# Kernel optimization log

Measured on AMD Instinct MI355X. Metric: run time of the kernel, lower is better.

Reference implementation:

```python
import jax, jax.numpy as jnp
import numpy as np

N, F, E, WID, M, K = 100000, 128, 128, 4, 25000, 16
HID = WID * F    # width * num_features = 512
DHID = WID * E   # discriminator hidden = 512
EPS = 1e-5


def _v2v(x, v_idx, w_e):
    """Hypergraph v2v mean aggregation: v->e mean (scaled by w_e), then e->v mean."""
    Mm, Kk = v_idx.shape
    C = x.shape[1]
    ef = jnp.zeros((Mm, C), x.dtype)
    for k in range(Kk):  # K is small and static; avoids a [M,K,C] materialization
        ef = ef + x[v_idx[:, k]]
    ef = ef * (w_e / Kk)[:, None]  # weighted edge features [M, C]
    out = jnp.zeros_like(x)
    deg = jnp.zeros((x.shape[0],), x.dtype)
    for k in range(Kk):
        out = out.at[v_idx[:, k]].add(ef)
        deg = deg.at[v_idx[:, k]].add(1.0)
    return out / jnp.maximum(deg, 1.0)[:, None]


def _bn(h, g, bt):
    # BatchNorm1d in training mode: biased batch stats over vertex dim
    m = h.mean(0)
    v = ((h - m) ** 2).mean(0)
    return g * (h - m) * jax.lax.rsqrt(v + EPS) + bt


def _conv(x, Wt, b, g, bt, v_idx, w_e, last=False):
    h = _bn(x @ Wt.T + b, g, bt)
    h = _v2v(h, v_idx, w_e)
    return h if last else jax.nn.relu(h)  # dropout = identity (eval mode)


def setup_inputs() -> dict:
    key = jax.random.key(0)
    ks = iter(jax.random.split(key, 64))

    def lin(o, i):
        s = 1.0 / np.sqrt(i)
        return (jax.random.uniform(next(ks), (o, i), minval=-s, maxval=s, dtype=jnp.float32),
                jax.random.uniform(next(ks), (o,), minval=-s, maxval=s, dtype=jnp.float32))

    d = {}
    d["X"] = jax.random.normal(next(ks), (N, F), dtype=jnp.float32)
    d["v_idx"] = jax.random.randint(next(ks), (M, K), 0, N, dtype=jnp.int32)
    d["w_e"] = jax.random.uniform(next(ks), (M,), dtype=jnp.float32)
    for name, (o, i) in [("enc1", (HID, F)), ("enc2", (E, HID)), ("fc", (E, HID)),
                         ("f1u", (E, E)), ("f2u", (E, E)), ("f1r", (E, E)), ("f2r", (E, E)),
                         ("f1", (E, E)), ("f2", (E, E)),
                         ("dis1", (DHID, E)), ("dis2", (2, DHID)),
                         ("dec1", (HID, E)), ("dec2", (F, HID))]:
        Wt, b = lin(o, i)
        d[name + "_W"] = Wt
        d[name + "_b"] = b
    for name, c in [("enc1", HID), ("enc2", E), ("dis1", DHID), ("dis2", 2), ("dec1", HID), ("dec2", F)]:
        d[name + "_g"] = jnp.ones((c,), jnp.float32)
        d[name + "_bt"] = jnp.zeros((c,), jnp.float32)
    return d


def reference(X, v_idx, w_e,
              enc1_W, enc1_b, enc2_W, enc2_b, fc_W, fc_b,
              f1u_W, f1u_b, f2u_W, f2u_b, f1r_W, f1r_b, f2r_W, f2r_b,
              f1_W, f1_b, f2_W, f2_b,
              dis1_W, dis1_b, dis2_W, dis2_b, dec1_W, dec1_b, dec2_W, dec2_b,
              enc1_g, enc1_bt, enc2_g, enc2_bt, dis1_g, dis1_bt, dis2_g, dis2_bt,
              dec1_g, dec1_bt, dec2_g, dec2_bt):
    # encoder (returns last output and first-layer output)
    x1 = _conv(X, enc1_W, enc1_b, enc1_g, enc1_bt, v_idx, w_e)            # [N, HID]
    xe = _conv(x1, enc2_W, enc2_b, enc2_g, enc2_bt, v_idx, w_e, last=True)  # [N, E]
    xe1 = x1 @ fc_W.T + fc_b                                               # [N, E]
    # GRU-style gating
    z = jax.nn.sigmoid(xe1 @ f1u_W.T + f1u_b + xe @ f2u_W.T + f2u_b)
    r = jax.nn.sigmoid(xe1 @ f1r_W.T + f1r_b + xe @ f2r_W.T + f2r_b)
    o = jnp.tanh(xe1 @ f1_W.T + f1_b + (r * xe) @ f2_W.T + f2_b)
    outs = z * o + (1.0 - z) * xe                                          # [N, E]
    # attention pooling (n = input_size - 1)
    dd = (outs - outs.mean(0)) ** 2
    vv = dd.sum(0) / (N - 1)
    ee = dd / (4.0 * (vv + 0.001)) + 0.5
    proto = (outs * jax.nn.sigmoid(ee)).sum(0)                             # [E]
    # gradient reversal is identity in the forward pass
    h = _conv(outs, dis1_W, dis1_b, dis1_g, dis1_bt, v_idx, w_e)
    xdis = _conv(h, dis2_W, dis2_b, dis2_g, dis2_bt, v_idx, w_e, last=True)  # [N, 2]
    h = _conv(outs, dec1_W, dec1_b, dec1_g, dec1_bt, v_idx, w_e)
    x_de = _conv(h, dec2_W, dec2_b, dec2_g, dec2_bt, v_idx, w_e, last=True)  # [N, F]
    return (outs, x_de, proto, xdis)
```

## Files before the change

### kernel.cpp

```cpp
#include <hip/hip_runtime.h>
#include <cstddef>
#include <cstdint>

static constexpr int NV = 100000;
static constexpr int NP = 100096;
static constexpr int ME = 25000;
static constexpr int MEP = 25088;
static constexpr int KE = 16;
static constexpr float BN_EPS = 1e-5f;

typedef unsigned int u32;
typedef __attribute__((ext_vector_type(8))) short s16x8;
typedef __attribute__((ext_vector_type(8))) unsigned short u16x8;
typedef __attribute__((ext_vector_type(4))) float f32x4;

__device__ __forceinline__ float sigm(float x) { return 1.0f / (1.0f + expf(-x)); }
__device__ __forceinline__ float bf2f(unsigned short u) {
    union { u32 i; float f; } v; v.i = ((u32)u) << 16; return v.f;
}
__device__ __forceinline__ unsigned short f2bf(float f) {
    union { float f; u32 i; } v; v.f = f;
    u32 u = v.i;
    return (unsigned short)((u + 0x7FFFu + ((u >> 16) & 1u)) >> 16);
}

#define GLD16(g, l) __builtin_amdgcn_global_load_lds(                          \
    (__attribute__((address_space(1))) const unsigned int*)(g),                \
    (__attribute__((address_space(3))) unsigned int*)(l), 16, 0, 0)

#define STAGE_A(b, k0)                                                         \
  {                                                                            \
    unsigned short* sA_ = sm + (b) * 8192;                                     \
    _Pragma("unroll")                                                          \
    for (int i_ = 0; i_ < 4; ++i_) {                                           \
      const unsigned short* g_ = A + (size_t)(bm + 32 * w + 8 * i_ + (l >> 3)) * IC + (k0) + swz; \
      GLD16(g_, sA_ + 2048 * w + 512 * i_);                                    \
    }                                                                          \
  }

__global__ __launch_bounds__(256)
void mfma_gemm(const unsigned short* __restrict__ A, int IC,
               const unsigned short* __restrict__ W, const float* __restrict__ bias,
               unsigned short* __restrict__ Cb, int ldb, int cb0,
               unsigned short* __restrict__ Cb2, int ldb2, int splitN,
               float* __restrict__ s1f, float* __restrict__ s2f, int statsC)
{
    __shared__ unsigned short sm[2 * 8192];
    const int BX = gridDim.x;
    const int total = BX * gridDim.y;
    const int flat = blockIdx.x + BX * blockIdx.y;
    const int q = total >> 3, r = total & 7;
    const int xcd = flat & 7, sub = flat >> 3;
    const int base = (xcd < r) ? xcd * (q + 1) : r * (q + 1) + (xcd - r) * q;
    const int vid = base + sub;
    const int bm = (vid / BX) * 128;
    const int bn = (vid % BX) * 64;

    const int tid = threadIdx.x;
    const int l = tid & 63, w = tid >> 6;
    const int wrow = w >> 1, wcol = w & 1;

    f32x4 acc[4][2];
    #pragma unroll
    for (int m = 0; m < 4; ++m)
        #pragma unroll
        for (int n = 0; n < 2; ++n)
            #pragma unroll
            for (int r2 = 0; r2 < 4; ++r2) acc[m][n][r2] = 0.f;

    const int swz = (((l & 7) ^ (l >> 3)) << 3);
    const int nt = IC >> 6;

    STAGE_A(0, 0);
    asm volatile("s_waitcnt vmcnt(0)" ::: "memory");
    __builtin_amdgcn_s_barrier();

    for (int t = 0; t < nt; ++t) {
        const int cur = t & 1;
        if (t + 1 < nt) STAGE_A(cur ^ 1, (t + 1) << 6);
        const unsigned short* sA = sm + cur * 8192;
        #pragma unroll
        for (int ks = 0; ks < 2; ++ks) {
            const int koff = ks * 32 + ((l >> 4) << 3);
            s16x8 afr[4], bfr[2];
            #pragma unroll
            for (int m = 0; m < 4; ++m) {
                int row = wrow * 64 + m * 16 + (l & 15);
                afr[m] = *(const s16x8*)&sA[row * 64 + (koff ^ ((l & 7) << 3))];
            }
            #pragma unroll
            for (int n = 0; n < 2; ++n) {
                int col = bn + wcol * 32 + n * 16 + (l & 15);
                bfr[n] = *(const s16x8*)&W[(size_t)col * IC + (t << 6) + koff];
            }
            #pragma unroll
            for (int m = 0; m < 4; ++m)
                #pragma unroll
                for (int n = 0; n < 2; ++n)
                    acc[m][n] = __builtin_amdgcn_mfma_f32_16x16x32_bf16(
                        afr[m], bfr[n], acc[m][n], 0, 0, 0);
        }
        asm volatile("s_waitcnt vmcnt(0)" ::: "memory");
        __builtin_amdgcn_s_barrier();
    }

    unsigned short* dst = Cb;
    int ld = ldb, co = cb0;
    if (Cb2 && bn >= splitN) { dst = Cb2; ld = ldb2; co = -splitN; }

    #pragma unroll
    for (int n = 0; n < 2; ++n) {
        const int col = bn + wcol * 32 + n * 16 + (l & 15);
        const float bs = bias[col];
        float ssum = 0.f, sq = 0.f;
        #pragma unroll
        for (int m = 0; m < 4; ++m) {
            const int row0 = bm + wrow * 64 + m * 16 + ((l >> 4) << 2);
            #pragma unroll
            for (int r2 = 0; r2 < 4; ++r2) {
                float v = acc[m][n][r2] + bs;
                int row = row0 + r2;
                if (dst) dst[(size_t)row * ld + co + col] = f2bf(v);
                if (s1f && col < statsC && row < NV) { ssum += v; sq += v * v; }
            }
        }
        if (s1f && col < statsC) {
            ssum += __shfl_xor(ssum, 16); ssum += __shfl_xor(ssum, 32);
            sq   += __shfl_xor(sq, 16);   sq   += __shfl_xor(sq, 32);
            if ((l >> 4) == 0) {
                atomicAdd(&s1f[col], ssum);
                atomicAdd(&s2f[col], sq);
            }
        }
    }
}

__global__ __launch_bounds__(256)
void mfma_gemm_ef2(const unsigned short* __restrict__ A,
                   const unsigned short* __restrict__ W,
                   const float* __restrict__ we,
                   const float* __restrict__ P, const float* __restrict__ Q,
                   unsigned short* __restrict__ ef0, unsigned short* __restrict__ ef1)
{
    const int IC = 128;
    __shared__ unsigned short sm[2 * 8192];
    const int bm = blockIdx.y * 128;
    const int bn = blockIdx.x * 64;
    const int tid = threadIdx.x;
    const int l = tid & 63, w = tid >> 6;
    const int wrow = w >> 1, wcol = w & 1;

    f32x4 acc[4][2];
    #pragma unroll
    for (int m = 0; m < 4; ++m)
        #pragma unroll
        for (int n = 0; n < 2; ++n)
            #pragma unroll
            for (int r = 0; r < 4; ++r) acc[m][n][r] = 0.f;

    const int swz = (((l & 7) ^ (l >> 3)) << 3);

    STAGE_A(0, 0);
    asm volatile("s_waitcnt vmcnt(0)" ::: "memory");
    __builtin_amdgcn_s_barrier();

    #pragma unroll
    for (int t = 0; t < 2; ++t) {
        const int cur = t & 1;
        if (t == 0) STAGE_A(1, 64);
        const unsigned short* sA = sm + cur * 8192;
        #pragma unroll
        for (int ks = 0; ks < 2; ++ks) {
            const int koff = ks * 32 + ((l >> 4) << 3);
            s16x8 afr[4], bfr[2];
            #pragma unroll
            for (int m = 0; m < 4; ++m) {
                int row = wrow * 64 + m * 16 + (l & 15);
                afr[m] = *(const s16x8*)&sA[row * 64 + (koff ^ ((l & 7) << 3))];
            }
            #pragma unroll
            for (int n = 0; n < 2; ++n) {
                int col = bn + wcol * 32 + n * 16 + (l & 15);
                bfr[n] = *(const s16x8*)&W[(size_t)col * 128 + (t << 6) + koff];
            }
            #pragma unroll
            for (int m = 0; m < 4; ++m)
                #pragma unroll
                for (int n = 0; n < 2; ++n)
                    acc[m][n] = __builtin_amdgcn_mfma_f32_16x16x32_bf16(
                        afr[m], bfr[n], acc[m][n], 0, 0, 0);
        }
        asm volatile("s_waitcnt vmcnt(0)" ::: "memory");
        __builtin_amdgcn_s_barrier();
    }

    unsigned short* dst = (bn < 512) ? ef0 : ef1;
    const int co = (bn < 512) ? 0 : -512;

    #pragma unroll
    for (int n = 0; n < 2; ++n) {
        const int colg = bn + wcol * 32 + n * 16 + (l & 15);
        const float pc = P[colg], qc = Q[colg];
        #pragma unroll
        for (int m = 0; m < 4; ++m) {
            const int row0 = bm + wrow * 64 + m * 16 + ((l >> 4) << 2);
            #pragma unroll
            for (int r = 0; r < 4; ++r) {
                int row = row0 + r;
                if (row < ME) {
                    float wv = we[row];
                    dst[(size_t)row * 512 + co + colg] = f2bf(wv * (pc * acc[m][n][r] + qc));
                }
            }
        }
    }
}

__global__ __launch_bounds__(256)
void cov_kernel(const unsigned short* __restrict__ A, float* __restrict__ cov)
{
    __shared__ unsigned short T[128 * 64];
    const int tid = threadIdx.x;
    const int l = tid & 63, w = tid >> 6;

    f32x4 acc[2][8];
    #pragma unroll
    for (int m = 0; m < 2; ++m)
        #pragma unroll
        for (int n = 0; n < 8; ++n)
            #pragma unroll
            for (int r = 0; r < 4; ++r) acc[m][n][r] = 0.f;

    const int r0 = blockIdx.x * 1024;
    for (int ch = 0; ch < 16; ++ch) {
        const int rbase = r0 + ch * 64;
        __syncthreads();
        #pragma unroll
        for (int q = 0; q < 4; ++q) {
            int idx = tid + q * 256;
            int r = idx & 63, cg = idx >> 6;
            int row = rbase + r;
            u16x8 u = {0, 0, 0, 0, 0, 0, 0, 0};
            if (row < NV) u = *(const u16x8*)&A[(size_t)row * 128 + cg * 8];
            #pragma unroll
            for (int j = 0; j < 8; ++j) {
                int c = cg * 8 + j;
                T[c * 64 + (r ^ ((c & 7) << 3))] = u[j];
            }
        }
        __syncthreads();
        #pragma unroll
        for (int ks = 0; ks < 2; ++ks) {
            const int koff = ks * 32 + ((l >> 4) << 3);
            s16x8 fi[2], fj[8];
            #pragma unroll
            for (int m = 0; m < 2; ++m) {
                int c = (w * 2 + m) * 16 + (l & 15);
                fi[m] = *(const s16x8*)&T[c * 64 + (koff ^ ((c & 7) << 3))];
            }
            #pragma unroll
            for (int n = 0; n < 8; ++n) {
                int c = n * 16 + (l & 15);
                fj[n] = *(const s16x8*)&T[c * 64 + (koff ^ ((c & 7) << 3))];
            }
            #pragma unroll
            for (int m = 0; m < 2; ++m)
                #pragma unroll
                for (int n = 0; n < 8; ++n)
                    acc[m][n] = __builtin_amdgcn_mfma_f32_16x16x32_bf16(
                        fi[m], fj[n], acc[m][n], 0, 0, 0);
        }
    }
    #pragma unroll
    for (int m = 0; m < 2; ++m) {
        #pragma unroll
        for (int n = 0; n < 8; ++n) {
            #pragma unroll
            for (int r = 0; r < 4; ++r) {
                int row = (w * 2 + m) * 16 + ((l >> 4) << 2) + r;
                int col = n * 16 + (l & 15);
                atomicAdd(&cov[row * 128 + col], acc[m][n][r]);
            }
        }
    }
}

__global__ __launch_bounds__(128)
void quadform_kernel(const float* __restrict__ cov, const float* __restrict__ colsum,
                     const unsigned short* __restrict__ Wt, const float* __restrict__ bias,
                     float* __restrict__ s1, float* __restrict__ s2)
{
    const int c = blockIdx.x, i = threadIdx.x;
    __shared__ float wv[128];
    __shared__ float red[128][2];
    float wi = bf2f(Wt[c * 128 + i]);
    wv[i] = wi;
    __syncthreads();
    const float* crow = cov + i * 128;
    float dot = 0.f;
    #pragma unroll 8
    for (int j = 0; j < 128; ++j) dot += crow[j] * wv[j];
    red[i][0] = wi * dot;
    red[i][1] = wi * colsum[i];
    __syncthreads();
    for (int s = 64; s > 0; s >>= 1) {
        if (i < s) { red[i][0] += red[i + s][0]; red[i][1] += red[i + s][1]; }
        __syncthreads();
    }
    if (i == 0) {
        float b = bias[c];
        float ws = red[0][1];
        s1[c] = ws + (float)NV * b;
        s2[c] = red[0][0] + 2.f * b * ws + (float)NV * b * b;
    }
}

__global__ void prep_weights(const float* e1, const float* e2, const float* fcw,
                             const float* d1, const float* dc1, const float* dc2,
                             const float* ds2,
                             const float* f1u, const float* f2u,
                             const float* f1r, const float* f2r,
                             const float* f1, const float* f2,
                             const float* f1ub, const float* f2ub,
                             const float* f1rb, const float* f2rb,
                             const float* f1b, const float* f2b,
                             const float* ds1b, const float* dc1b,
                             const float* e2b, const float* fcb,
                             unsigned short* WB, float* bzr, float* bo,
                             float* bdd, float* bef)
{
    int i = blockIdx.x * 256 + threadIdx.x;
    if (i < 65536)           WB[i] = f2bf(e1[i]);
    else if (i < 131072)     WB[i] = f2bf(e2[i - 65536]);
    else if (i < 196608)     WB[i] = f2bf(fcw[i - 131072]);
    else if (i < 262144)     WB[i] = f2bf(d1[i - 196608]);
    else if (i < 327680)     WB[i] = f2bf(dc1[i - 262144]);
    else if (i < 393216)     WB[i] = f2bf(dc2[i - 327680]);
    else if (i < 394240)     WB[i] = f2bf(ds2[i - 393216]);
    else if (i < 459776) {
        int j = i - 394240, row = j >> 8, c = j & 255;
        float v;
        if (row < 128) v = (c < 128) ? f1u[row * 128 + c] : f2u[row * 128 + c - 128];
        else { int rr = row - 128; v = (c < 128) ? f1r[rr * 128 + c] : f2r[rr * 128 + c - 128]; }
        WB[i] = f2bf(v);
    } else if (i < 492544) {
        int j = i - 459776, row = j >> 8, c = j & 255;
        float v = (c < 128) ? f1[row * 128 + c] : f2[row * 128 + c - 128];
        WB[i] = f2bf(v);
    } else if (i < 492800) {
        int o = i - 492544;
        bzr[o] = (o < 128) ? (f1ub[o] + f2ub[o]) : (f1rb[o - 128] + f2rb[o - 128]);
    } else if (i < 492928) {
        int o = i - 492800;
        bo[o] = f1b[o] + f2b[o];
    } else if (i < 493952) {
        int o = i - 492928;
        bdd[o] = (o < 512) ? ds1b[o] : dc1b[o - 512];
    } else if (i < 494208) {
        int o = i - 493952;
        bef[o] = (o < 128) ? e2b[o] : fcb[o - 128];
    }
}

__global__ void cvt_f32_bf16(const float* __restrict__ in, unsigned short* __restrict__ out, int n)
{
    int i = (blockIdx.x * 256 + threadIdx.x) * 4;
    if (i < n) {
        float4 v = *reinterpret_cast<const float4*>(&in[i]);
        out[i] = f2bf(v.x); out[i + 1] = f2bf(v.y);
        out[i + 2] = f2bf(v.z); out[i + 3] = f2bf(v.w);
    }
}

__global__ void bn_finalize_kernel(const float* __restrict__ s1, const float* __restrict__ s2,
                                   const float* __restrict__ g, const float* __restrict__ bt,
                                   float* __restrict__ scale, float* __restrict__ shift,
                                   int C, float invN)
{
    int c = threadIdx.x;
    if (c < C) {
        float m = s1[c] * invN;
        float v = fmaxf(s2[c] * invN - m * m, 0.f);
        float sc = g[c] * rsqrtf(v + BN_EPS);
        scale[c] = sc;
        shift[c] = bt[c] - m * sc;
    }
}

__global__ void bn_finalize_pq(const float* __restrict__ s1, const float* __restrict__ s2,
                               const float* __restrict__ g, const float* __restrict__ bt,
                               const float* __restrict__ bias,
                               float* __restrict__ P, float* __restrict__ Q,
                               int C, int off, float invN)
{
    int c = threadIdx.x;
    if (c < C) {
        int cc = off + c;
        float m = s1[cc] * invN;
        float v = fmaxf(s2[cc] * invN - m * m, 0.f);
        float sc = g[c] * rsqrtf(v + BN_EPS);
        float sh = bt[c] - m * sc;
        P[cc] = sc * (1.0f / KE);
        Q[cc] = sc * bias[c] + sh;
    }
}

__global__ __launch_bounds__(256)
void edge_gather_sum(const unsigned short* __restrict__ x, const int* __restrict__ vidx,
                     unsigned short* __restrict__ ge)
{
    const int e = blockIdx.x * 16 + (threadIdx.x >> 4);
    const int cp = (threadIdx.x & 15) << 3;
    if (e >= ME) return;
    float s[8] = {};
    const int* vi = vidx + e * KE;
    #pragma unroll
    for (int k = 0; k < KE; ++k) {
        int v = vi[k];
        u16x8 u = *(const u16x8*)&x[(size_t)v * 128 + cp];
        #pragma unroll
        for (int j = 0; j < 8; ++j) s[j] += bf2f(u[j]);
    }
    u16x8 o;
    #pragma unroll
    for (int j = 0; j < 8; ++j) o[j] = f2bf(s[j]);
    *(u16x8*)&ge[(size_t)e * 128 + cp] = o;
}

__global__ __launch_bounds__(256)
void edge_gather_bf(const unsigned short* __restrict__ pre, const int* __restrict__ vidx,
                    const float* __restrict__ we, const float* __restrict__ scl,
                    const float* __restrict__ shf, unsigned short* __restrict__ ef, int C)
{
    const int tpe = C >> 3;
    const int epb = 256 / tpe;
    const int e = blockIdx.x * epb + threadIdx.x / tpe;
    const int cp = (threadIdx.x % tpe) << 3;
    if (e >= ME) return;
    float s[8] = {};
    const int* vi = vidx + e * KE;
    #pragma unroll
    for (int k = 0; k < KE; ++k) {
        int v = vi[k];
        u16x8 u = *(const u16x8*)&pre[(size_t)v * C + cp];
        #pragma unroll
        for (int j = 0; j < 8; ++j) s[j] += bf2f(u[j]);
    }
    float wv = we[e] * (1.0f / KE);
    u16x8 o;
    #pragma unroll
    for (int j = 0; j < 8; ++j)
        o[j] = f2bf(wv * (scl[cp + j] * s[j] + (float)KE * shf[cp + j]));
    *(u16x8*)&ef[(size_t)e * C + cp] = o;
}

__global__ void edge_gather2_kernel(const float* __restrict__ X, const int* __restrict__ vidx,
                                    const float* __restrict__ we, const float* __restrict__ scale,
                                    const float* __restrict__ shift, float* __restrict__ ef)
{
    int e = blockIdx.x * blockDim.x + threadIdx.x;
    if (e >= ME) return;
    float s0 = 0.f, s1v = 0.f;
    #pragma unroll
    for (int k = 0; k < KE; ++k) {
        int v = vidx[e * KE + k];
        s0 += X[2 * v];
        s1v += X[2 * v + 1];
    }
    float w = we[e] * (1.0f / KE);
    ef[2 * e]     = w * (scale[0] * s0 + (float)KE * shift[0]);
    ef[2 * e + 1] = w * (scale[1] * s1v + (float)KE * shift[1]);
}

__global__ void deg_kernel(const int* __restrict__ vidx, int* __restrict__ deg)
{
    int i = blockIdx.x * blockDim.x + threadIdx.x;
    if (i < ME * KE) atomicAdd(&deg[vidx[i]], 1);
}

__global__ void scan_block_kernel(const int* __restrict__ deg, int* __restrict__ rowptr,
                                  int* __restrict__ blocksums, int n)
{
    __shared__ int tmp[256];
    int i = blockIdx.x * 256 + threadIdx.x;
    int v = (i < n) ? deg[i] : 0;
    tmp[threadIdx.x] = v;
    __syncthreads();
    for (int off = 1; off < 256; off <<= 1) {
        int t = (threadIdx.x >= off) ? tmp[threadIdx.x - off] : 0;
        __syncthreads();
        tmp[threadIdx.x] += t;
        __syncthreads();
    }
    if (i < n) rowptr[i] = tmp[threadIdx.x] - v;
    if (threadIdx.x == 255) blocksums[blockIdx.x] = tmp[255];
}

__global__ void scan_sums_par(int* __restrict__ bs, int nb)
{
    __shared__ int tmp[512];
    int t = threadIdx.x;
    int v = (t < nb) ? bs[t] : 0;
    tmp[t] = v;
    __syncthreads();
    for (int off = 1; off < 512; off <<= 1) {
        int u = (t >= off) ? tmp[t - off] : 0;
        __syncthreads();
        tmp[t] += u;
        __syncthreads();
    }
    if (t < nb) bs[t] = tmp[t] - v;
}

__global__ void scan_add_kernel(int* __restrict__ rowptr, const int* __restrict__ blocksums, int n)
{
    int i = blockIdx.x * 256 + threadIdx.x;
    if (i < n) rowptr[i] += blocksums[blockIdx.x];
    if (i == 0) rowptr[n] = ME * KE;
}

__global__ void csr_fill_kernel(const int* __restrict__ vidx, int* __restrict__ cursor,
                                int* __restrict__ csr)
{
    int i = blockIdx.x * blockDim.x + threadIdx.x;
    if (i < ME * KE) {
        int v = vidx[i];
        int pos = atomicAdd(&cursor[v], 1);
        csr[pos] = i >> 4;
    }
}

__global__ __launch_bounds__(256)
void csr_gather_bf(const unsigned short* __restrict__ ef, int ldE, int cb0E,
                   const int* __restrict__ rowptr, const int* __restrict__ csr,
                   float* __restrict__ outf, int ldf,
                   unsigned short* __restrict__ outb, int ldb, int cb0,
                   unsigned short* __restrict__ outb2, int ldb2,
                   int C, int relu)
{
    const int lpv = C >> 3;
    const int vpb = 256 / lpv;
    const int v = blockIdx.x * vpb + threadIdx.x / lpv;
    const int lg = threadIdx.x % lpv;
    if (v >= NV) return;
    const int s = rowptr[v], e = rowptr[v + 1];
    float a[8] = {};
    int i = s;
    for (; i + 2 <= e; i += 2) {
        int e0 = csr[i], e1 = csr[i + 1];
        u16x8 u0 = *(const u16x8*)&ef[(size_t)e0 * ldE + cb0E + lg * 8];
        u16x8 u1 = *(const u16x8*)&ef[(size_t)e1 * ldE + cb0E + lg * 8];
        #pragma unroll
        for (int j = 0; j < 8; ++j) a[j] += bf2f(u0[j]) + bf2f(u1[j]);
    }
    if (i < e) {
        int e0 = csr[i];
        u16x8 u0 = *(const u16x8*)&ef[(size_t)e0 * ldE + cb0E + lg * 8];
        #pragma unroll
        for (int j = 0; j < 8; ++j) a[j] += bf2f(u0[j]);
    }
    float inv = 1.0f / (float)max(e - s, 1);
    #pragma unroll
    for (int j = 0; j < 8; ++j) {
        float x = a[j] * inv;
        if (relu) x = fmaxf(x, 0.f);
        a[j] = x;
    }
    if (outf) {
        float* p = outf + (size_t)v * ldf + lg * 8;
        #pragma unroll
        for (int j = 0; j < 8; ++j) p[j] = a[j];
    }
    if (outb) {
        u16x8 o;
        #pragma unroll
        for (int j = 0; j < 8; ++j) o[j] = f2bf(a[j]);
        *(u16x8*)&outb[(size_t)v * ldb + cb0 + lg * 8] = o;
    }
    if (outb2) {
        u16x8 o;
        #pragma unroll
        for (int j = 0; j < 8; ++j) o[j] = f2bf(a[j]);
        *(u16x8*)&outb2[(size_t)v * ldb2 + lg * 8] = o;
    }
}

__global__ __launch_bounds__(256)
void csr_gather_dis(const unsigned short* __restrict__ ef,
                    const int* __restrict__ rowptr, const int* __restrict__ csr,
                    const unsigned short* __restrict__ wdis2, const float* __restrict__ dis2b,
                    float* __restrict__ pre22)
{
    const int w = threadIdx.x >> 6, l = threadIdx.x & 63;
    const int v = blockIdx.x * 4 + w;
    if (v >= NV) return;
    const int s = rowptr[v], e = rowptr[v + 1];
    float a[8] = {};
    int i = s;
    for (; i + 2 <= e; i += 2) {
        int e0 = csr[i], e1 = csr[i + 1];
        u16x8 u0 = *(const u16x8*)&ef[(size_t)e0 * 512 + l * 8];
        u16x8 u1 = *(const u16x8*)&ef[(size_t)e1 * 512 + l * 8];
        #pragma unroll
        for (int j = 0; j < 8; ++j) a[j] += bf2f(u0[j]) + bf2f(u1[j]);
    }
    if (i < e) {
        int e0 = csr[i];
        u16x8 u0 = *(const u16x8*)&ef[(size_t)e0 * 512 + l * 8];
        #pragma unroll
        for (int j = 0; j < 8; ++j) a[j] += bf2f(u0[j]);
    }
    float inv = 1.0f / (float)max(e - s, 1);
    u16x8 w0 = *(const u16x8*)&wdis2[l * 8];
    u16x8 w1 = *(const u16x8*)&wdis2[512 + l * 8];
    float d0 = 0.f, d1 = 0.f;
    #pragma unroll
    for (int j = 0; j < 8; ++j) {
        float h = fmaxf(a[j] * inv, 0.f);
        d0 += h * bf2f(w0[j]);
        d1 += h * bf2f(w1[j]);
    }
    for (int o = 32; o > 0; o >>= 1) {
        d0 += __shfl_down(d0, o);
        d1 += __shfl_down(d1, o);
    }
    if (l == 0) {
        pre22[2 * v]     = d0 + dis2b[0];
        pre22[2 * v + 1] = d1 + dis2b[1];
    }
}

__global__ void csr_gather2_kernel(const float* __restrict__ ef, const int* __restrict__ rowptr,
                                   const int* __restrict__ csr, float* __restrict__ outp)
{
    int v = blockIdx.x * blockDim.x + threadIdx.x;
    if (v >= NV) return;
    int s = rowptr[v], e = rowptr[v + 1];
    float a0 = 0.f, a1 = 0.f;
    for (int i = s; i < e; ++i) {
        int ed = csr[i];
        a0 += ef[2 * ed];
        a1 += ef[2 * ed + 1];
    }
    float inv = 1.0f / (float)max(e - s, 1);
    outp[2 * v]     = a0 * inv;
    outp[2 * v + 1] = a1 * inv;
}

__global__ __launch_bounds__(256)
void colstats_bf(const unsigned short* __restrict__ Xb,
                 float* __restrict__ s1, float* __restrict__ s2)
{
    const int t = threadIdx.x;
    const int cg = t & 15;
    const int rs = t >> 4;
    float s[8] = {}, q[8] = {};
    for (int r = blockIdx.x * 16 + rs; r < NV; r += 256 * 16) {
        u16x8 u = *(const u16x8*)&Xb[(size_t)r * 128 + cg * 8];
        #pragma unroll
        for (int j = 0; j < 8; ++j) {
            float v = bf2f(u[j]);
            s[j] += v; q[j] += v * v;
        }
    }
    __shared__ float ls[16][16][8];
    __shared__ float lq[16][16][8];
    #pragma unroll
    for (int j = 0; j < 8; ++j) { ls[rs][cg][j] = s[j]; lq[rs][cg][j] = q[j]; }
    __syncthreads();
    int c = t & 127;
    float a = 0.f;
    if (t < 128) {
        #pragma unroll
        for (int i = 0; i < 16; ++i) a += ls[i][c >> 3][c & 7];
        atomicAdd(&s1[c], a);
    } else {
        #pragma unroll
        for (int i = 0; i < 16; ++i) a += lq[i][c >> 3][c & 7];
        atomicAdd(&s2[c], a);
    }
}

__global__ void att_finalize_kernel(const float* __restrict__ s1, const float* __restrict__ s2,
                                    float* __restrict__ mu, float* __restrict__ qd, int C)
{
    int c = threadIdx.x;
    if (c < C) {
        float m = s1[c] / (float)NV;
        float vv = fmaxf((s2[c] - (float)NV * m * m) / (float)(NV - 1), 0.f);
        mu[c] = m;
        qd[c] = 1.0f / (4.0f * (vv + 0.001f));
    }
}

__global__ __launch_bounds__(256)
void proto_ws(const float* __restrict__ outsf, const float* __restrict__ mu,
              const float* __restrict__ qd, float* __restrict__ proto)
{
    const int t = threadIdx.x;
    const int cg = t & 31;
    const int rs = t >> 5;
    const float4* X4 = (const float4*)outsf;
    const float4 m = ((const float4*)mu)[cg];
    const float4 q = ((const float4*)qd)[cg];
    float4 acc = make_float4(0.f, 0.f, 0.f, 0.f);
    for (int r = blockIdx.x * 8 + rs; r < NV; r += 256 * 8) {
        float4 x = X4[(size_t)r * 32 + cg];
        float d0 = (x.x - m.x) * (x.x - m.x);
        float d1 = (x.y - m.y) * (x.y - m.y);
        float d2 = (x.z - m.z) * (x.z - m.z);
        float d3 = (x.w - m.w) * (x.w - m.w);
        acc.x += x.x * sigm(d0 * q.x + 0.5f);
        acc.y += x.y * sigm(d1 * q.y + 0.5f);
        acc.z += x.z * sigm(d2 * q.z + 0.5f);
        acc.w += x.w * sigm(d3 * q.w + 0.5f);
    }
    __shared__ float4 ls[8][32];
    ls[rs][cg] = acc;
    __syncthreads();
    if (t < 128) {
        float a = 0.f;
        #pragma unroll
        for (int i = 0; i < 8; ++i) {
            const float* f = (const float*)&ls[i][t >> 2];
            a += f[t & 3];
        }
        atomicAdd(&proto[t], a);
    }
}

__global__ void colstats2_kernel(const float* __restrict__ X, int N,
                                 float* __restrict__ s1, float* __restrict__ s2)
{
    __shared__ float red[256][4];
    int t = threadIdx.x;
    float a0 = 0, a1 = 0, b0 = 0, b1 = 0;
    for (int r = blockIdx.x * 256 + t; r < N; r += 256 * gridDim.x) {
        float x0 = X[2 * r], x1 = X[2 * r + 1];
        a0 += x0; b0 += x0 * x0;
        a1 += x1; b1 += x1 * x1;
    }
    red[t][0] = a0; red[t][1] = a1; red[t][2] = b0; red[t][3] = b1;
    __syncthreads();
    for (int s = 128; s > 0; s >>= 1) {
        if (t < s)
            for (int j = 0; j < 4; ++j) red[t][j] += red[t + s][j];
        __syncthreads();
    }
    if (t == 0) {
        atomicAdd(&s1[0], red[0][0]);
        atomicAdd(&s1[1], red[0][1]);
        atomicAdd(&s2[0], red[0][2]);
        atomicAdd(&s2[1], red[0][3]);
    }
}

__global__ void rx_kernel(const unsigned short* __restrict__ ZR, const unsigned short* __restrict__ xeb,
                          unsigned short* __restrict__ G, int n8)
{
    int idx = blockIdx.x * blockDim.x + threadIdx.x;
    if (idx >= n8) return;
    int i8 = idx * 8;
    int row = i8 >> 7, c = i8 & 127;
    u16x8 rv = *(const u16x8*)&ZR[(size_t)row * 256 + 128 + c];
    u16x8 xv = *(const u16x8*)&xeb[i8];
    u16x8 g;
    #pragma unroll
    for (int j = 0; j < 8; ++j)
        g[j] = f2bf(sigm(bf2f(rv[j])) * bf2f(xv[j]));
    *(u16x8*)&G[(size_t)row * 256 + 128 + c] = g;
}

__global__ void gru_out_kernel(const unsigned short* __restrict__ ZR, const unsigned short* __restrict__ Opre,
                               const unsigned short* __restrict__ xeb,
                               float* __restrict__ outs, unsigned short* __restrict__ outsb,
                               float* __restrict__ outsf, int n8)
{
    int idx = blockIdx.x * blockDim.x + threadIdx.x;
    if (idx >= n8) return;
    int i8 = idx * 8;
    int row = i8 >> 7, c = i8 & 127;
    u16x8 zv = *(const u16x8*)&ZR[(size_t)row * 256 + c];
    u16x8 ov = *(const u16x8*)&Opre[i8];
    u16x8 xv = *(const u16x8*)&xeb[i8];
    float val[8];
    u16x8 ob;
    #pragma unroll
    for (int j = 0; j < 8; ++j) {
        float z = sigm(bf2f(zv[j]));
        float o = tanhf(bf2f(ov[j]));
        float xe = bf2f(xv[j]);
        val[j] = z * o + (1.f - z) * xe;
        ob[j] = f2bf(val[j]);
    }
    *(float4*)&outs[i8]     = make_float4(val[0], val[1], val[2], val[3]);
    *(float4*)&outs[i8 + 4] = make_float4(val[4], val[5], val[6], val[7]);
    *(float4*)&outsf[i8]     = make_float4(val[0], val[1], val[2], val[3]);
    *(float4*)&outsf[i8 + 4] = make_float4(val[4], val[5], val[6], val[7]);
    *(u16x8*)&outsb[i8] = ob;
}

extern "C" void kernel_launch(void* const* d_in, const int* in_sizes, int n_in,
                              void* d_out, int out_size, void* d_ws, size_t ws_size,
                              hipStream_t stream)
{
    const float* X      = (const float*)d_in[0];
    const int*   vidx   = (const int*)  d_in[1];
    const float* we     = (const float*)d_in[2];
    const float* enc1_W = (const float*)d_in[3];  const float* enc1_b = (const float*)d_in[4];
    const float* enc2_W = (const float*)d_in[5];  const float* enc2_b = (const float*)d_in[6];
    const float* fc_W   = (const float*)d_in[7];  const float* fc_b   = (const float*)d_in[8];
    const float* f1u_W  = (const float*)d_in[9];  const float* f1u_b  = (const float*)d_in[10];
    const float* f2u_W  = (const float*)d_in[11]; const float* f2u_b  = (const float*)d_in[12];
    const float* f1r_W  = (const float*)d_in[13]; const float* f1r_b  = (const float*)d_in[14];
    const float* f2r_W  = (const float*)d_in[15]; const float* f2r_b  = (const float*)d_in[16];
    const float* f1_W   = (const float*)d_in[17]; const float* f1_b   = (const float*)d_in[18];
    const float* f2_W   = (const float*)d_in[19]; const float* f2_b   = (const float*)d_in[20];
    const float* dis1_W = (const float*)d_in[21]; const float* dis1_b = (const float*)d_in[22];
    const float* dis2_W = (const float*)d_in[23]; const float* dis2_b = (const float*)d_in[24];
    const float* dec1_W = (const float*)d_in[25]; const float* dec1_b = (const float*)d_in[26];
    const float* dec2_W = (const float*)d_in[27]; const float* dec2_b = (const float*)d_in[28];
    const float* enc1_g = (const float*)d_in[29]; const float* enc1_bt = (const float*)d_in[30];
    const float* enc2_g = (const float*)d_in[31]; const float* enc2_bt = (const float*)d_in[32];
    const float* dis1_g = (const float*)d_in[33]; const float* dis1_bt = (const float*)d_in[34];
    const float* dis2_g = (const float*)d_in[35]; const float* dis2_bt = (const float*)d_in[36];
    const float* dec1_g = (const float*)d_in[37]; const float* dec1_bt = (const float*)d_in[38];
    const float* dec2_g = (const float*)d_in[39]; const float* dec2_bt = (const float*)d_in[40];

    float* out   = (float*)d_out;
    float* outs  = out;
    float* x_de  = out + 12800000;
    float* proto = out + 25600000;
    float* xdis  = out + 25600128;

    char* base = (char*)d_ws;
    unsigned short* bufA = (unsigned short*)base;
    char* p = base + (size_t)NP * 512 * 2;
    unsigned short* bufE = (unsigned short*)p; p += (size_t)MEP * 1024 * 2;
    unsigned short* Greg = (unsigned short*)p;
    unsigned short* Xbf  = Greg;
    unsigned short* outsb = Greg + (size_t)NP * 128;
    p += (size_t)NP * 256 * 2;
    unsigned short* x1bf = (unsigned short*)p; p += (size_t)NP * 512 * 2;
    unsigned short* WB = (unsigned short*)p; p += 492544 * 2 + 1024;
    float* bzr = (float*)p; p += 256 * 4;
    float* bo  = (float*)p; p += 128 * 4;
    float* bdd = (float*)p; p += 1024 * 4;
    float* bef = (float*)p; p += 256 * 4;
    float* s1  = (float*)p; p += 1024 * 4;
    float* s2  = (float*)p; p += 1024 * 4;
    float* scl = (float*)p; p += 1024 * 4;
    float* shf = (float*)p; p += 1024 * 4;
    float* sX1 = (float*)p; p += 128 * 4;
    float* sX2 = (float*)p; p += 128 * 4;
    float* sA1 = (float*)p; p += 128 * 4;
    float* sA2 = (float*)p; p += 128 * 4;
    float* covX = (float*)p; p += 16384 * 4;
    float* covA = (float*)p; p += 16384 * 4;
    int* deg    = (int*)p; p += (size_t)NV * 4;
    int* rowptr = (int*)p; p += (size_t)(NV + 1) * 4;
    int* cursor = (int*)p; p += (size_t)NV * 4;
    int* bsums  = (int*)p; p += 512 * 4;
    int* csr    = (int*)p; p += (size_t)ME * KE * 4;
    float* outsf = (float*)p; p += (size_t)NP * 128 * 4;
    unsigned short* ge = (unsigned short*)p;

    unsigned short* bufE0 = bufE;
    unsigned short* bufE1 = bufE + (size_t)MEP * 512;

    unsigned short* pre128 = bufA;
    unsigned short* xe_bf  = bufA + (size_t)NP * 128;
    unsigned short* ZR     = bufA + (size_t)NP * 256;
    unsigned short* Opre   = bufA;
    unsigned short* hdec   = bufA;
    float* pre22 = (float*)(Greg + (size_t)NP * 128);
    float* bufEf = (float*)bufE;

    unsigned short* wenc1 = WB;
    unsigned short* wenc2 = WB + 65536;
    unsigned short* wdd   = WB + 196608;
    unsigned short* wdec2 = WB + 327680;
    unsigned short* wdis2 = WB + 393216;
    unsigned short* wzr   = WB + 394240;
    unsigned short* wo    = WB + 459776;

    const int n128 = NV * 128;
    const int n8 = n128 / 8;
    const int nScanBlocks = (NV + 255) / 256;

    auto gemm = [&](const unsigned short* A, int ic, const unsigned short* W, const float* b,
                    unsigned short* Cb, int ldb, int cb0,
                    unsigned short* Cb2, int ldb2, int splitN,
                    int oc, float* st1, float* st2, int statsC) {
        dim3 g(oc / 64, NP / 128);
        mfma_gemm<<<g, 256, 0, stream>>>(A, ic, W, b, Cb, ldb, cb0, Cb2, ldb2, splitN,
                                         st1, st2, statsC);
    };

    prep_weights<<<1931, 256, 0, stream>>>(enc1_W, enc2_W, fc_W, dis1_W, dec1_W, dec2_W, dis2_W,
                                           f1u_W, f2u_W, f1r_W, f2r_W, f1_W, f2_W,
                                           f1u_b, f2u_b, f1r_b, f2r_b, f1_b, f2_b,
                                           dis1_b, dec1_b, enc2_b, fc_b,
                                           WB, bzr, bo, bdd, bef);
    cvt_f32_bf16<<<(n128 / 4 + 255) / 256, 256, 0, stream>>>(X, Xbf, n128);

    hipMemsetAsync(deg, 0, NV * sizeof(int), stream);
    deg_kernel<<<(ME * KE + 255) / 256, 256, 0, stream>>>(vidx, deg);
    scan_block_kernel<<<nScanBlocks, 256, 0, stream>>>(deg, rowptr, bsums, NV);
    scan_sums_par<<<1, 512, 0, stream>>>(bsums, nScanBlocks);
    scan_add_kernel<<<nScanBlocks, 256, 0, stream>>>(rowptr, bsums, NV);
    hipMemcpyAsync(cursor, rowptr, NV * sizeof(int), hipMemcpyDeviceToDevice, stream);
    csr_fill_kernel<<<(ME * KE + 255) / 256, 256, 0, stream>>>(vidx, cursor, csr);

    hipMemsetAsync(sX1, 0, 256 * sizeof(float), stream);
    hipMemsetAsync(covX, 0, 16384 * sizeof(float), stream);
    colstats_bf<<<256, 256, 0, stream>>>(Xbf, sX1, sX2);
    cov_kernel<<<98, 256, 0, stream>>>(Xbf, covX);
    quadform_kernel<<<512, 128, 0, stream>>>(covX, sX1, wenc1, enc1_b, s1, s2);
    bn_finalize_pq<<<1, 512, 0, stream>>>(s1, s2, enc1_g, enc1_bt, enc1_b, scl, shf, 512, 0, 1.0f / NV);
    edge_gather_sum<<<(ME + 15) / 16, 256, 0, stream>>>(Xbf, vidx, ge);
    { dim3 g(8, MEP / 128);
      mfma_gemm_ef2<<<g, 256, 0, stream>>>(ge, wenc1, we, scl, shf, bufE0, bufE1); }
    csr_gather_bf<<<NV / 4, 256, 0, stream>>>(bufE0, 512, 0, rowptr, csr,
        nullptr, 0, x1bf, 512, 0, nullptr, 0, 512, 1);

    hipMemsetAsync(s1, 0, 2048 * sizeof(float), stream);
    gemm(x1bf, 512, wenc2, bef, pre128, 128, 0, Greg, 256, 128, 256, s1, s2, 128);
    bn_finalize_kernel<<<1, 512, 0, stream>>>(s1, s2, enc2_g, enc2_bt, scl, shf, 128, 1.0f / NV);
    edge_gather_bf<<<(ME + 15) / 16, 256, 0, stream>>>(pre128, vidx, we, scl, shf, bufE0, 128);
    csr_gather_bf<<<NV / 16, 256, 0, stream>>>(bufE0, 128, 0, rowptr, csr,
        nullptr, 0, Greg, 256, 128, xe_bf, 128, 128, 0);

    gemm(Greg, 256, wzr, bzr, ZR, 256, 0, nullptr, 0, 1 << 30, 256, nullptr, nullptr, 0);
    rx_kernel<<<(n8 + 255) / 256, 256, 0, stream>>>(ZR, xe_bf, Greg, n8);
    gemm(Greg, 256, wo, bo, Opre, 128, 0, nullptr, 0, 1 << 30, 128, nullptr, nullptr, 0);
    gru_out_kernel<<<(n8 + 255) / 256, 256, 0, stream>>>(ZR, Opre, xe_bf, outs, outsb, outsf, n8);

    hipMemsetAsync(sA1, 0, 256 * sizeof(float), stream);
    colstats_bf<<<256, 256, 0, stream>>>(outsb, sA1, sA2);
    att_finalize_kernel<<<1, 128, 0, stream>>>(sA1, sA2, scl, shf, 128);
    hipMemsetAsync(proto, 0, 128 * sizeof(float), stream);
    proto_ws<<<256, 256, 0, stream>>>(outsf, scl, shf, proto);

    hipMemsetAsync(covA, 0, 16384 * sizeof(float), stream);
    cov_kernel<<<98, 256, 0, stream>>>(outsb, covA);
    quadform_kernel<<<1024, 128, 0, stream>>>(covA, sA1, wdd, bdd, s1, s2);
    bn_finalize_pq<<<1, 512, 0, stream>>>(s1, s2, dis1_g, dis1_bt, dis1_b, scl, shf, 512, 0, 1.0f / NV);
    bn_finalize_pq<<<1, 512, 0, stream>>>(s1, s2, dec1_g, dec1_bt, dec1_b, scl, shf, 512, 512, 1.0f / NV);
    edge_gather_sum<<<(ME + 15) / 16, 256, 0, stream>>>(outsb, vidx, ge);
    { dim3 g(16, MEP / 128);
      mfma_gemm_ef2<<<g, 256, 0, stream>>>(ge, wdd, we, scl, shf, bufE0, bufE1); }
    csr_gather_dis<<<NV / 4, 256, 0, stream>>>(bufE0, rowptr, csr, wdis2, dis2_b, pre22);
    csr_gather_bf<<<NV / 4, 256, 0, stream>>>(bufE1, 512, 0, rowptr, csr,
        nullptr, 0, hdec, 512, 0, nullptr, 0, 512, 1);

    hipMemsetAsync(s1, 0, 2048 * sizeof(float), stream);
    colstats2_kernel<<<64, 256, 0, stream>>>(pre22, NV, s1, s2);
    bn_finalize_kernel<<<1, 512, 0, stream>>>(s1, s2, dis2_g, dis2_bt, scl, shf, 2, 1.0f / NV);
    edge_gather2_kernel<<<(ME + 255) / 256, 256, 0, stream>>>(pre22, vidx, we, scl, shf, bufEf);
    csr_gather2_kernel<<<(NV + 255) / 256, 256, 0, stream>>>(bufEf, rowptr, csr, xdis);

    hipMemsetAsync(s1, 0, 2048 * sizeof(float), stream);
    gemm(hdec, 512, wdec2, dec2_b, Greg, 128, 0, nullptr, 0, 1 << 30, 128, s1, s2, 128);
    bn_finalize_kernel<<<1, 512, 0, stream>>>(s1, s2, dec2_g, dec2_bt, scl, shf, 128, 1.0f / NV);
    edge_gather_bf<<<(ME + 15) / 16, 256, 0, stream>>>(Greg, vidx, we, scl, shf, bufE0, 128);
    csr_gather_bf<<<NV / 16, 256, 0, stream>>>(bufE0, 128, 0, rowptr, csr,
        x_de, 128, nullptr, 0, 0, nullptr, 0, 128, 0);
}
```

Before: 890.8 us.

## Fuse GRU gating elementwise kernels into GEMM epilogues with split-A staging

The separate rx_kernel and gru_out_kernel are removed. Their sigmoid/tanh/blend math now runs in the epilogues of the z/r GEMM and the output GEMM. The GEMM gains a two-source A operand so the output GEMM can read [xe1 | r*xe] from two buffers without writing a concatenated matrix. The ef2 GEMM also adopts the XCD-aware block swizzle. This cuts full-size intermediate round trips and two launches, but the fused epilogues do scalar strided stores and extra per-element loads.

```diff
diff --git a/kernel.cpp b/kernel.cpp
--- a/kernel.cpp
+++ b/kernel.cpp
@@ -28,22 +28,28 @@
     (__attribute__((address_space(1))) const unsigned int*)(g),                \
     (__attribute__((address_space(3))) unsigned int*)(l), 16, 0, 0)
 
-#define STAGE_A(b, k0)                                                         \
+#define STAGE_G(b, SRC, LD, k0)                                                \
   {                                                                            \
     unsigned short* sA_ = sm + (b) * 8192;                                     \
     _Pragma("unroll")                                                          \
     for (int i_ = 0; i_ < 4; ++i_) {                                           \
-      const unsigned short* g_ = A + (size_t)(bm + 32 * w + 8 * i_ + (l >> 3)) * IC + (k0) + swz; \
+      const unsigned short* g_ = (SRC) + (size_t)(bm + 32 * w + 8 * i_ + (l >> 3)) * (LD) + (k0) + swz; \
       GLD16(g_, sA_ + 2048 * w + 512 * i_);                                    \
     }                                                                          \
   }
 
 __global__ __launch_bounds__(256)
-void mfma_gemm(const unsigned short* __restrict__ A, int IC,
+void mfma_gemm(const unsigned short* __restrict__ A, int ldA, int IC1,
+               const unsigned short* __restrict__ A2, int ldA2, int IC,
                const unsigned short* __restrict__ W, const float* __restrict__ bias,
                unsigned short* __restrict__ Cb, int ldb, int cb0,
                unsigned short* __restrict__ Cb2, int ldb2, int splitN,
-               float* __restrict__ s1f, float* __restrict__ s2f, int statsC)
+               float* __restrict__ s1f, float* __restrict__ s2f, int statsC,
+               int fuse, const unsigned short* __restrict__ xe_p,
+               const unsigned short* __restrict__ zbuf,
+               unsigned short* __restrict__ rxout,
+               float* __restrict__ o_outs, float* __restrict__ o_outsf,
+               unsigned short* __restrict__ o_outsb)
 {
     __shared__ unsigned short sm[2 * 8192];
     const int BX = gridDim.x;
@@ -71,13 +77,18 @@
     const int swz = (((l & 7) ^ (l >> 3)) << 3);
     const int nt = IC >> 6;
 
-    STAGE_A(0, 0);
+    #define STAGE_T(b, t)                                                      \
+      { int k0_ = (t) << 6;                                                    \
+        if (k0_ < IC1) { STAGE_G(b, A, ldA, k0_) }                             \
+        else           { STAGE_G(b, A2, ldA2, k0_ - IC1) } }
+
+    STAGE_T(0, 0);
     asm volatile("s_waitcnt vmcnt(0)" ::: "memory");
     __builtin_amdgcn_s_barrier();
 
     for (int t = 0; t < nt; ++t) {
         const int cur = t & 1;
-        if (t + 1 < nt) STAGE_A(cur ^ 1, (t + 1) << 6);
+        if (t + 1 < nt) STAGE_T(cur ^ 1, t + 1);
         const unsigned short* sA = sm + cur * 8192;
         #pragma unroll
         for (int ks = 0; ks < 2; ++ks) {
@@ -102,6 +113,55 @@
         }
         asm volatile("s_waitcnt vmcnt(0)" ::: "memory");
         __builtin_amdgcn_s_barrier();
+    }
+    #undef STAGE_T
+
+    if (fuse == 1) {
+        #pragma unroll
+        for (int n = 0; n < 2; ++n) {
+            const int col = bn + wcol * 32 + n * 16 + (l & 15);
+            const float bs = bias[col];
+            #pragma unroll
+            for (int m = 0; m < 4; ++m) {
+                const int row0 = bm + wrow * 64 + m * 16 + ((l >> 4) << 2);
+                #pragma unroll
+                for (int r2 = 0; r2 < 4; ++r2) {
+                    const int row = row0 + r2;
+                    float v = acc[m][n][r2] + bs;
+                    if (col < 128) {
+                        Cb[(size_t)row * 128 + col] = f2bf(v);
+                    } else {
+                        float xe = bf2f(xe_p[(size_t)row * 128 + col - 128]);
+                        rxout[(size_t)row * 128 + col - 128] = f2bf(sigm(v) * xe);
+                    }
+                }
+            }
+        }
+        return;
+    }
+    if (fuse == 2) {
+        #pragma unroll
+        for (int n = 0; n < 2; ++n) {
+            const int col = bn + wcol * 32 + n * 16 + (l & 15);
+            const float bs = bias[col];
+            #pragma unroll
+            for (int m = 0; m < 4; ++m) {
+                const int row0 = bm + wrow * 64 + m * 16 + ((l >> 4) << 2);
+                #pragma unroll
+                for (int r2 = 0; r2 < 4; ++r2) {
+                    const int row = row0 + r2;
+                    if (row < NV) {
+                        float z = sigm(bf2f(zbuf[(size_t)row * 128 + col]));
+                        float xe = bf2f(xe_p[(size_t)row * 128 + col]);
+                        float val = z * tanhf(acc[m][n][r2] + bs) + (1.f - z) * xe;
+                        o_outs[(size_t)row * 128 + col] = val;
+                        o_outsf[(size_t)row * 128 + col] = val;
+                        o_outsb[(size_t)row * 128 + col] = f2bf(val);
+                    }
+                }
+            }
+        }
+        return;
     }
 
     unsigned short* dst = Cb;
@@ -142,10 +202,18 @@
                    const float* __restrict__ P, const float* __restrict__ Q,
                    unsigned short* __restrict__ ef0, unsigned short* __restrict__ ef1)
 {
-    const int IC = 128;
+    const int ldA = 128;
     __shared__ unsigned short sm[2 * 8192];
-    const int bm = blockIdx.y * 128;
-    const int bn = blockIdx.x * 64;
+    const int BX = gridDim.x;
+    const int total = BX * gridDim.y;
+    const int flat = blockIdx.x + BX * blockIdx.y;
+    const int q = total >> 3, rr = total & 7;
+    const int xcd = flat & 7, sub = flat >> 3;
+    const int base = (xcd < rr) ? xcd * (q + 1) : rr * (q + 1) + (xcd - rr) * q;
+    const int vid = base + sub;
+    const int bm = (vid / BX) * 128;
+    const int bn = (vid % BX) * 64;
+
     const int tid = threadIdx.x;
     const int l = tid & 63, w = tid >> 6;
     const int wrow = w >> 1, wcol = w & 1;
@@ -160,14 +228,14 @@
 
     const int swz = (((l & 7) ^ (l >> 3)) << 3);
 
-    STAGE_A(0, 0);
+    STAGE_G(0, A, ldA, 0);
     asm volatile("s_waitcnt vmcnt(0)" ::: "memory");
     __builtin_amdgcn_s_barrier();
 
     #pragma unroll
     for (int t = 0; t < 2; ++t) {
         const int cur = t & 1;
-        if (t == 0) STAGE_A(1, 64);
+        if (t == 0) STAGE_G(1, A, ldA, 64);
         const unsigned short* sA = sm + cur * 8192;
         #pragma unroll
         for (int ks = 0; ks < 2; ++ks) {
@@ -755,51 +823,6 @@
     }
 }
 
-__global__ void rx_kernel(const unsigned short* __restrict__ ZR, const unsigned short* __restrict__ xeb,
-                          unsigned short* __restrict__ G, int n8)
-{
-    int idx = blockIdx.x * blockDim.x + threadIdx.x;
-    if (idx >= n8) return;
-    int i8 = idx * 8;
-    int row = i8 >> 7, c = i8 & 127;
-    u16x8 rv = *(const u16x8*)&ZR[(size_t)row * 256 + 128 + c];
-    u16x8 xv = *(const u16x8*)&xeb[i8];
-    u16x8 g;
-    #pragma unroll
-    for (int j = 0; j < 8; ++j)
-        g[j] = f2bf(sigm(bf2f(rv[j])) * bf2f(xv[j]));
-    *(u16x8*)&G[(size_t)row * 256 + 128 + c] = g;
-}
-
-__global__ void gru_out_kernel(const unsigned short* __restrict__ ZR, const unsigned short* __restrict__ Opre,
-                               const unsigned short* __restrict__ xeb,
-                               float* __restrict__ outs, unsigned short* __restrict__ outsb,
-                               float* __restrict__ outsf, int n8)
-{
-    int idx = blockIdx.x * blockDim.x + threadIdx.x;
-    if (idx >= n8) return;
-    int i8 = idx * 8;
-    int row = i8 >> 7, c = i8 & 127;
-    u16x8 zv = *(const u16x8*)&ZR[(size_t)row * 256 + c];
-    u16x8 ov = *(const u16x8*)&Opre[i8];
-    u16x8 xv = *(const u16x8*)&xeb[i8];
-    float val[8];
-    u16x8 ob;
-    #pragma unroll
-    for (int j = 0; j < 8; ++j) {
-        float z = sigm(bf2f(zv[j]));
-        float o = tanhf(bf2f(ov[j]));
-        float xe = bf2f(xv[j]);
-        val[j] = z * o + (1.f - z) * xe;
-        ob[j] = f2bf(val[j]);
-    }
-    *(float4*)&outs[i8]     = make_float4(val[0], val[1], val[2], val[3]);
-    *(float4*)&outs[i8 + 4] = make_float4(val[4], val[5], val[6], val[7]);
-    *(float4*)&outsf[i8]     = make_float4(val[0], val[1], val[2], val[3]);
-    *(float4*)&outsf[i8 + 4] = make_float4(val[4], val[5], val[6], val[7]);
-    *(u16x8*)&outsb[i8] = ob;
-}
-
 extern "C" void kernel_launch(void* const* d_in, const int* in_sizes, int n_in,
                               void* d_out, int out_size, void* d_ws, size_t ws_size,
                               hipStream_t stream)
@@ -839,7 +862,6 @@
     unsigned short* bufE = (unsigned short*)p; p += (size_t)MEP * 1024 * 2;
     unsigned short* Greg = (unsigned short*)p;
     unsigned short* Xbf  = Greg;
-    unsigned short* outsb = Greg + (size_t)NP * 128;
     p += (size_t)NP * 256 * 2;
     unsigned short* x1bf = (unsigned short*)p; p += (size_t)NP * 512 * 2;
     unsigned short* WB = (unsigned short*)p; p += 492544 * 2 + 1024;
@@ -870,9 +892,10 @@
 
     unsigned short* pre128 = bufA;
     unsigned short* xe_bf  = bufA + (size_t)NP * 128;
-    unsigned short* ZR     = bufA + (size_t)NP * 256;
-    unsigned short* Opre   = bufA;
+    unsigned short* ZRz    = bufA + (size_t)NP * 256;
     unsigned short* hdec   = bufA;
+    unsigned short* RX     = x1bf;
+    unsigned short* outsb  = x1bf + (size_t)NP * 128;
     float* pre22 = (float*)(Greg + (size_t)NP * 128);
     float* bufEf = (float*)bufE;
 
@@ -885,16 +908,22 @@
     unsigned short* wo    = WB + 459776;
 
     const int n128 = NV * 128;
-    const int n8 = n128 / 8;
     const int nScanBlocks = (NV + 255) / 256;
 
-    auto gemm = [&](const unsigned short* A, int ic, const unsigned short* W, const float* b,
+    auto gemm = [&](const unsigned short* A, int ldA, int ic1,
+                    const unsigned short* A2, int ldA2, int ic,
+                    const unsigned short* W, const float* b,
                     unsigned short* Cb, int ldb, int cb0,
                     unsigned short* Cb2, int ldb2, int splitN,
-                    int oc, float* st1, float* st2, int statsC) {
+                    int oc, float* st1, float* st2, int statsC,
+                    int fuse, const unsigned short* xe_p,
+                    const unsigned short* zbuf, unsigned short* rxout,
+                    float* oo, float* oof, unsigned short* oob) {
         dim3 g(oc / 64, NP / 128);
-        mfma_gemm<<<g, 256, 0, stream>>>(A, ic, W, b, Cb, ldb, cb0, Cb2, ldb2, splitN,
-                                         st1, st2, statsC);
+        mfma_gemm<<<g, 256, 0, stream>>>(A, ldA, ic1, A2, ldA2, ic, W, b,
+                                         Cb, ldb, cb0, Cb2, ldb2, splitN,
+                                         st1, st2, statsC, fuse, xe_p, zbuf,
+                                         rxout, oo, oof, oob);
     };
 
     prep_weights<<<1931, 256, 0, stream>>>(enc1_W, enc2_W, fc_W, dis1_W, dec1_W, dec2_W, dis2_W,
@@ -925,16 +954,20 @@
         nullptr, 0, x1bf, 512, 0, nullptr, 0, 512, 1);
 
     hipMemsetAsync(s1, 0, 2048 * sizeof(float), stream);
-    gemm(x1bf, 512, wenc2, bef, pre128, 128, 0, Greg, 256, 128, 256, s1, s2, 128);
+    gemm(x1bf, 512, 512, nullptr, 0, 512, wenc2, bef, pre128, 128, 0,
+         Greg, 256, 128, 256, s1, s2, 128, 0, nullptr, nullptr, nullptr,
+         nullptr, nullptr, nullptr);
     bn_finalize_kernel<<<1, 512, 0, stream>>>(s1, s2, enc2_g, enc2_bt, scl, shf, 128, 1.0f / NV);
     edge_gather_bf<<<(ME + 15) / 16, 256, 0, stream>>>(pre128, vidx, we, scl, shf, bufE0, 128);
     csr_gather_bf<<<NV / 16, 256, 0, stream>>>(bufE0, 128, 0, rowptr, csr,
         nullptr, 0, Greg, 256, 128, xe_bf, 128, 128, 0);
 
-    gemm(Greg, 256, wzr, bzr, ZR, 256, 0, nullptr, 0, 1 << 30, 256, nullptr, nullptr, 0);
-    rx_kernel<<<(n8 + 255) / 256, 256, 0, stream>>>(ZR, xe_bf, Greg, n8);
-    gemm(Greg, 256, wo, bo, Opre, 128, 0, nullptr, 0, 1 << 30, 128, nullptr, nullptr, 0);
-    gru_out_kernel<<<(n8 + 255) / 256, 256, 0, stream>>>(ZR, Opre, xe_bf, outs, outsb, outsf, n8);
+    gemm(Greg, 256, 256, nullptr, 0, 256, wzr, bzr, ZRz, 128, 0,
+         nullptr, 0, 1 << 30, 256, nullptr, nullptr, 0,
+         1, xe_bf, nullptr, RX, nullptr, nullptr, nullptr);
+    gemm(Greg, 256, 128, RX, 128, 256, wo, bo, nullptr, 0, 0,
+         nullptr, 0, 1 << 30, 128, nullptr, nullptr, 0,
+         2, xe_bf, ZRz, nullptr, outs, outsf, outsb);
 
     hipMemsetAsync(sA1, 0, 256 * sizeof(float), stream);
     colstats_bf<<<256, 256, 0, stream>>>(outsb, sA1, sA2);
@@ -961,7 +994,9 @@
     csr_gather2_kernel<<<(NV + 255) / 256, 256, 0, stream>>>(bufEf, rowptr, csr, xdis);
 
     hipMemsetAsync(s1, 0, 2048 * sizeof(float), stream);
-    gemm(hdec, 512, wdec2, dec2_b, Greg, 128, 0, nullptr, 0, 1 << 30, 128, s1, s2, 128);
+    gemm(hdec, 512, 512, nullptr, 0, 512, wdec2, dec2_b, Greg, 128, 0,
+         nullptr, 0, 1 << 30, 128, s1, s2, 128, 0, nullptr, nullptr, nullptr,
+         nullptr, nullptr, nullptr);
     bn_finalize_kernel<<<1, 512, 0, stream>>>(s1, s2, dec2_g, dec2_bt, scl, shf, 128, 1.0f / NV);
     edge_gather_bf<<<(ME + 15) / 16, 256, 0, stream>>>(Greg, vidx, we, scl, shf, bufE0, 128);
     csr_gather_bf<<<NV / 16, 256, 0, stream>>>(bufE0, 128, 0, rowptr, csr,
```

Result: slower. 917.4 us (+3.0%).
